# Kernel tuning notes

Measured on AMD Instinct MI355X. Metric: run time of the kernel, lower is better.

Reference implementation:

```python
import jax, jax.numpy as jnp
import numpy as np

HIDDEN = 2048
HEADS = 16
HEAD_DIM = HIDDEN // HEADS
ROPE_BASE = 10000.0


def rope_cos_sin(seq_len, dim, dtype=jnp.float32):
    inv_freq = 1.0 / (ROPE_BASE ** (jnp.arange(0, dim, 2, dtype=jnp.float32) / dim))
    t = jnp.arange(seq_len, dtype=jnp.float32)
    freqs = jnp.einsum('i,j->ij', t, inv_freq)            # [S, dim/2]
    emb = jnp.concatenate([freqs, freqs], axis=-1)        # [S, dim]
    return jnp.cos(emb).astype(dtype), jnp.sin(emb).astype(dtype)


def rotate_half(x):
    x1, x2 = jnp.split(x, 2, axis=-1)
    return jnp.concatenate([-x2, x1], axis=-1)


def setup_inputs() -> dict:
    key = jax.random.key(0)
    ks = jax.random.split(key, 6)
    B, S, D = 2, 2048, HIDDEN
    scale = 1.0 / np.sqrt(D)
    x = jax.random.normal(ks[0], (B, S, D), dtype=jnp.float32)
    Wq = jax.random.normal(ks[1], (D, D), dtype=jnp.float32) * scale
    Wk = jax.random.normal(ks[2], (D, D), dtype=jnp.float32) * scale
    Wv = jax.random.normal(ks[3], (D, D), dtype=jnp.float32) * scale
    Wo = jax.random.normal(ks[4], (D, D), dtype=jnp.float32) * scale
    bo = jnp.zeros((D,), dtype=jnp.float32)
    return {"x": x, "Wq": Wq, "Wk": Wk, "Wv": Wv, "Wo": Wo, "bo": bo}


def reference(x, Wq, Wk, Wv, Wo, bo):
    B, S, D = x.shape
    H, Dh = HEADS, HEAD_DIM
    # torch Linear: x @ W.T
    q = (x @ Wq.T).reshape(B, S, H, Dh).transpose(0, 2, 1, 3)  # [B,H,S,Dh]
    k = (x @ Wk.T).reshape(B, S, H, Dh).transpose(0, 2, 1, 3)
    v = (x @ Wv.T).reshape(B, S, H, Dh).transpose(0, 2, 1, 3)
    cos, sin = rope_cos_sin(S, Dh, x.dtype)                    # [S, Dh]
    q = q * cos + rotate_half(q) * sin
    k = k * cos + rotate_half(k) * sin
    scale = Dh ** -0.5
    attn = jnp.einsum('bhqd,bhkd->bhqk', q, k) * scale
    attn = jax.nn.softmax(attn, axis=-1)
    out = jnp.einsum('bhqk,bhkd->bhqd', attn, v)               # [B,H,S,Dh]
    out = out.transpose(0, 2, 1, 3).reshape(B, S, D)
    return out @ Wo.T + bo
```

## Files before the change

kernel.cpp:

```cpp
#include <hip/hip_runtime.h>
#include <stdint.h>


#define SEQ 2048
#define HD 128
#define DMODEL 2048

typedef __bf16 bf16x8 __attribute__((ext_vector_type(8)));
typedef float f32x4 __attribute__((ext_vector_type(4)));
typedef unsigned short u16;
typedef unsigned int u32;

typedef bf16x8 __attribute__((may_alias)) bf16x8_a;
typedef uint2 __attribute__((may_alias)) uint2_a;
typedef uint4 __attribute__((may_alias)) uint4_a;

__device__ __forceinline__ u16 f2bf(float f) {
  unsigned int u = __float_as_uint(f);
  u += 0x7fff + ((u >> 16) & 1);
  return (u16)(u >> 16);
}

typedef __attribute__((address_space(1))) void* gas_t;
typedef __attribute__((address_space(3))) void* las_t;
__device__ __forceinline__ void load_lds16(const void* g, void* l) {
  __builtin_amdgcn_global_load_lds((gas_t)(uintptr_t)g,
                                   (las_t)(uint32_t)(uintptr_t)l, 16, 0, 0);
}

__global__ void conv_all(const float* __restrict__ x,
                         const float* __restrict__ wq,
                         const float* __restrict__ wk,
                         const float* __restrict__ wv,
                         const float* __restrict__ wo,
                         u16* __restrict__ xb, u16* __restrict__ wqkv,
                         u16* __restrict__ wob) {
  int i = blockIdx.x * 256 + threadIdx.x;
  const float* src;
  u16* dst;
  int off;
  if (i < 2097152) { src = x; dst = xb; off = i; }
  else if (i < 3145728) { src = wq; dst = wqkv; off = i - 2097152; }
  else if (i < 4194304) { src = wk; dst = wqkv + 4194304; off = i - 3145728; }
  else if (i < 5242880) { src = wv; dst = wqkv + 8388608; off = i - 4194304; }
  else { src = wo; dst = wob; off = i - 5242880; }
  float4 v = ((const float4*)src)[off];
  ushort4 o;
  o.x = f2bf(v.x); o.y = f2bf(v.y); o.z = f2bf(v.z); o.w = f2bf(v.w);
  ((ushort4*)dst)[off] = o;
}


#define BARR asm volatile("s_barrier" ::: "memory")
#define LGKM0 asm volatile("s_waitcnt lgkmcnt(0)" ::: "memory")
#define VMW2 asm volatile("s_waitcnt vmcnt(2)" ::: "memory")
#define VMW8 asm volatile("s_waitcnt vmcnt(8)" ::: "memory")
#define VMW0 asm volatile("s_waitcnt vmcnt(0)" ::: "memory")

#define STGA(D, KOFF) do {                                                  \
    const u16* ga_ = Ag + (KOFF);                                           \
    u16* la_ = S + (D) * 16384;                                             \
    load_lds16(ga_ + off[0], la_ + tid * 8);                                \
    load_lds16(ga_ + off[1], la_ + (tid + 512) * 8);                        \
    load_lds16(ga_ + off[2], la_ + (tid + 1024) * 8);                       \
    load_lds16(ga_ + off[3], la_ + (tid + 1536) * 8);                       \
  } while (0)

#define STGB(D, KOFF) do {                                                  \
    const u16* gb_ = Bg + (KOFF);                                           \
    u16* lb_ = S + 32768 + (D) * 8192;                                      \
    load_lds16(gb_ + off[0], lb_ + tid * 8);                                \
    load_lds16(gb_ + off[1], lb_ + (tid + 512) * 8);                        \
  } while (0)

#define LDA2(D, MH) do {                                                    \
    const u16* ab_ = S + (D) * 16384;                                       \
    _Pragma("unroll") for (int mt_ = 0; mt_ < 2; ++mt_) {                   \
      int rA_ = wm * 64 + ((MH) * 2 + mt_) * 16 + l15;                      \
      int sw_ = rA_ & 7;                                                    \
      af[mt_][0] = *(const bf16x8_a*)(ab_ + (rA_ * 8 + (quad ^ sw_)) * 8);  \
      af[mt_][1] = *(const bf16x8_a*)(ab_ + (rA_ * 8 + ((4 + quad) ^ sw_)) * 8); \
    } } while (0)

#define LDB2(D) do {                                                        \
    const u16* bb_ = S + 32768 + (D) * 8192;                                \
    _Pragma("unroll") for (int nt_ = 0; nt_ < 4; ++nt_) {                   \
      int rB_ = wn * 64 + nt_ * 16 + l15;                                   \
      int sw_ = rB_ & 7;                                                    \
      bfr[nt_][0] = *(const bf16x8_a*)(bb_ + (rB_ * 8 + (quad ^ sw_)) * 8); \
      bfr[nt_][1] = *(const bf16x8_a*)(bb_ + (rB_ * 8 + ((4 + quad) ^ sw_)) * 8); \
    } } while (0)

#define MM2(MH) do {                                                        \
    __builtin_amdgcn_s_setprio(1);                                          \
    _Pragma("unroll") for (int c_ = 0; c_ < 2; ++c_)                        \
      _Pragma("unroll") for (int mt_ = 0; mt_ < 2; ++mt_)                   \
        _Pragma("unroll") for (int nt_ = 0; nt_ < 4; ++nt_) {               \
          if (VM)                                                           \
            acc[(MH) * 2 + mt_][nt_] =                                      \
                __builtin_amdgcn_mfma_f32_16x16x32_bf16(                    \
                    bfr[nt_][c_], af[mt_][c_],                              \
                    acc[(MH) * 2 + mt_][nt_], 0, 0, 0);                     \
          else                                                              \
            acc[(MH) * 2 + mt_][nt_] =                                      \
                __builtin_amdgcn_mfma_f32_16x16x32_bf16(                    \
                    af[mt_][c_], bfr[nt_][c_],                              \
                    acc[(MH) * 2 + mt_][nt_], 0, 0, 0);                     \
        }                                                                   \
    __builtin_amdgcn_s_setprio(0);                                          \
  } while (0)

template <bool VM>
__device__ __forceinline__ void mm_core(const u16* __restrict__ Ag,
                                        const u16* __restrict__ Bg,
                                        u16* __restrict__ S, int tid,
                                        f32x4 acc[4][4]) {
  const int lane = tid & 63;
  const int wave = tid >> 6;
  const int quad = lane >> 4;
  const int l15 = lane & 15;
  const int wm = wave >> 1;
  const int wn = wave & 1;

  u32 off[4];
#pragma unroll
  for (int j = 0; j < 4; ++j) {
    int idx = tid + j * 512;
    int r = idx >> 3;
    off[j] = (u32)r * 2048u + (u32)(((idx & 7) ^ (r & 7)) * 8);
  }

  bf16x8 af[2][2], bfr[4][2];

  STGA(0, 0);
  STGB(0, 0);
  STGB(1, 64);
  VMW2;
  BARR;

#pragma unroll 2
  for (int t = 0; t < 32; ++t) {
    const int d = t & 1;
    LDA2(d, 0); LDB2(d);
    if (t < 31) STGA(1 - d, (t + 1) * 64);
    BARR; LGKM0; MM2(0); BARR;
    LDA2(d, 1);
    if (t < 30) STGB(d, (t + 2) * 64);
    BARR; LGKM0; MM2(1);
    if (t < 30) { VMW2; } else if (t == 30) { VMW0; }
    BARR;
  }
}

__global__ __launch_bounds__(512, 2)
void gemm_qkv(const u16* __restrict__ A, const u16* __restrict__ Bm,
              u16* __restrict__ qkv, u16* __restrict__ vt) {
  __shared__ __align__(16) u16 S[49152];

  const int tid = threadIdx.x;
  int hwid = blockIdx.y * 48 + blockIdx.x;
  int logical = (hwid & 7) * 96 + (hwid >> 3);
  const int bx = logical >> 4;
  const int by = logical & 15;
  const int row0 = by * 256;
  const int col0 = bx * 128;
  const bool vmode = bx >= 32;

  const u16* Ag = A + (size_t)row0 * 2048;
  const u16* Bg = Bm + (size_t)col0 * 2048;

  f32x4 acc[4][4] = {};
  if (vmode) mm_core<true>(Ag, Bg, S, tid, acc);
  else       mm_core<false>(Ag, Bg, S, tid, acc);

  const int lane = tid & 63;
  const int wave = tid >> 6;
  const int quad = lane >> 4;
  const int l15 = lane & 15;
  const int wm = wave >> 1;
  const int wn = wave & 1;

  const int which = bx >> 4;
  const int h = bx & 15;
  const int brow = row0 >> 11;
  const int sbase = row0 & 2047;
  const float qs = (which == 0) ? 0.12751744f : 1.0f;

#pragma unroll
  for (int mt = 0; mt < 4; ++mt)
#pragma unroll
    for (int nt = 0; nt < 4; ++nt)
#pragma unroll
      for (int r = 0; r < 4; ++r) {
        int el;
        if (vmode) {
          int dd = wn * 64 + nt * 16 + quad * 4 + r;
          int ss = wm * 64 + mt * 16 + l15;
          el = dd * 256 + (((ss >> 3) ^ (dd & 31)) * 8) + (ss & 7);
        } else {
          int ss = wm * 64 + mt * 16 + quad * 4 + r;
          int dd = wn * 64 + nt * 16 + l15;
          el = ss * 128 + (((dd >> 3) ^ (ss & 15)) * 8) + (dd & 7);
        }
        S[el] = f2bf(acc[mt][nt][r] * qs);
      }
  __syncthreads();

  if (!vmode) {
    const int a = lane & 7;
    const int sg = lane >> 3;
    const float c1 = 0.2076205059304601f;
    const float c2 = 2.6514961294723187f;
#pragma unroll
    for (int pass = 0; pass < 4; ++pass) {
      int s_l = pass * 64 + wave * 8 + sg;
      int s2048 = sbase + s_l;
      int sw = s_l & 15;
      bf16x8 x1 = *(const bf16x8_a*)&S[s_l * 128 + ((a ^ sw) * 8)];
      bf16x8 x2 = *(const bf16x8_a*)&S[s_l * 128 + (((a + 8) ^ sw) * 8)];
      u16 o1[8], o2[8];
#pragma unroll
      for (int e = 0; e < 8; ++e) {
        float j = (float)(a * 8 + e);
        float rev = (float)s2048 * __builtin_amdgcn_exp2f(-c1 * j - c2);
        rev = __builtin_amdgcn_fractf(rev);
        float sn = __builtin_amdgcn_sinf(rev);
        float cs = __builtin_amdgcn_cosf(rev);
        float v1 = (float)x1[e], v2 = (float)x2[e];
        o1[e] = f2bf(v1 * cs - v2 * sn);
        o2[e] = f2bf(v2 * cs + v1 * sn);
      }
      size_t base =
          ((((size_t)which * 2 + brow) * 16 + h) * SEQ + s2048) * HD + a * 8;
      *(uint4_a*)&qkv[base] = *(uint4*)o1;
      *(uint4_a*)&qkv[base + 64] = *(uint4*)o2;
    }
  } else {
    const int d_part = tid >> 4;
    const int a0 = tid & 15;
#pragma unroll
    for (int pass = 0; pass < 4; ++pass) {
      int d_l = pass * 32 + d_part;
      int dw = d_l & 31;
      size_t rb = (((size_t)brow * 16 + h) * HD + d_l) * SEQ + sbase;
#pragma unroll
      for (int g = 0; g < 2; ++g) {
        int a2 = a0 + g * 16;
        bf16x8 y = *(const bf16x8_a*)&S[d_l * 256 + ((a2 ^ dw) * 8)];
        *(uint4_a*)&vt[rb + a2 * 8] = *(uint4_a*)&y;
      }
    }
  }
}

__global__ __launch_bounds__(512, 2)
void gemm_out(const u16* __restrict__ A, const u16* __restrict__ Bm,
              float* __restrict__ C, const float* __restrict__ bias) {
  __shared__ __align__(16) u16 S[49152];

  const int tid = threadIdx.x;
  int hwid = blockIdx.y * 16 + blockIdx.x;
  int logical = (hwid & 7) * 32 + (hwid >> 3);
  const int bx = logical >> 4;
  const int by = logical & 15;
  const int row0 = by * 256;
  const int col0 = bx * 128;

  const u16* Ag = A + (size_t)row0 * 2048;
  const u16* Bg = Bm + (size_t)col0 * 2048;

  f32x4 acc[4][4] = {};
  mm_core<false>(Ag, Bg, S, tid, acc);

  const int lane = tid & 63;
  const int wave = tid >> 6;
  const int quad = lane >> 4;
  const int l15 = lane & 15;
  const int wm = wave >> 1;
  const int wn = wave & 1;

#pragma unroll
  for (int nt = 0; nt < 4; ++nt) {
    int d = col0 + wn * 64 + nt * 16 + l15;
    float bv = bias[d];
#pragma unroll
    for (int mt = 0; mt < 4; ++mt) {
#pragma unroll
      for (int r = 0; r < 4; ++r) {
        int row = row0 + wm * 64 + mt * 16 + quad * 4 + r;
        C[(size_t)row * DMODEL + d] = acc[mt][nt][r] + bv;
      }
    }
  }
}

__global__ __launch_bounds__(256, 2)
void attn_kernel(const u16* __restrict__ qkv, const u16* __restrict__ vt,
                 u16* __restrict__ attn_out) {
  __shared__ __align__(16) u16 Kl[2][64 * 128];
  __shared__ __align__(16) u16 Vl[2][128 * 64];
  __shared__ __align__(16) u16 Pl[4][32 * 64];

  const int tid = threadIdx.x;
  const int lane = tid & 63;
  const int wave = tid >> 6;
  const int quad = lane >> 4;
  const int l15 = lane & 15;
  const int q0 = blockIdx.x * 128;
  const int bh = blockIdx.y;
  const size_t SD = (size_t)SEQ * HD;

  const u16* Q = qkv + (size_t)bh * SD;
  const u16* Kg = qkv + (size_t)(32 + bh) * SD;
  const u16* Vg = vt + (size_t)bh * SD;

  bf16x8 onesf;
#pragma unroll
  for (int e = 0; e < 8; ++e)
    onesf[e] = (l15 == 0) ? (__bf16)1.0f : (__bf16)0.0f;

  bf16x8 qf[2][4];
#pragma unroll
  for (int mt = 0; mt < 2; ++mt) {
    int qrow = q0 + wave * 32 + mt * 16 + l15;
#pragma unroll
    for (int c = 0; c < 4; ++c)
      qf[mt][c] = *(const bf16x8*)(Q + (size_t)qrow * HD + c * 32 + quad * 8);
  }

  f32x4 of[9][2] = {};
  u16* pw = &Pl[wave][0];

  auto stage = [&](int tile, int buf) {
    int kv0 = tile * 64;
#pragma unroll
    for (int j = 0; j < 4; ++j) {
      int idx = (wave * 4 + j) * 64 + lane;
      {
        int r = idx >> 4, cs = idx & 15;
        int cc = cs ^ (r & 15);
        load_lds16(Kg + (size_t)(kv0 + r) * HD + cc * 8, &Kl[buf][idx * 8]);
      }
      {
        int r = idx >> 3, cs = idx & 7;
        int cc = cs ^ (r & 7);
        load_lds16(Vg + (size_t)r * SEQ + kv0 + cc * 8, &Vl[buf][idx * 8]);
      }
    }
  };

  stage(0, 0);
  stage(1, 1);
  VMW8;
  BARR;

#pragma unroll 2
  for (int t = 0; t < 32; ++t) {
    const u16* Kb = Kl[t & 1];
    const u16* Vb = Vl[t & 1];

    f32x4 sc[4][2] = {};
    __builtin_amdgcn_s_setprio(1);
#pragma unroll
    for (int c = 0; c < 4; ++c) {
      bf16x8 kf[4];
#pragma unroll
      for (int nt = 0; nt < 4; ++nt)
        kf[nt] = *(const bf16x8*)&Kb[((nt * 16 + l15) * 16 +
                                      ((c * 4 + quad) ^ l15)) * 8];
#pragma unroll
      for (int nt = 0; nt < 4; ++nt)
#pragma unroll
        for (int mt = 0; mt < 2; ++mt)
          sc[nt][mt] = __builtin_amdgcn_mfma_f32_16x16x32_bf16(
              kf[nt], qf[mt][c], sc[nt][mt], 0, 0, 0);
    }
    __builtin_amdgcn_s_setprio(0);

#pragma unroll
    for (int nt = 0; nt < 4; ++nt) {
#pragma unroll
      for (int mt = 0; mt < 2; ++mt) {
        float p0 = __builtin_amdgcn_exp2f(sc[nt][mt][0]);
        float p1 = __builtin_amdgcn_exp2f(sc[nt][mt][1]);
        float p2 = __builtin_amdgcn_exp2f(sc[nt][mt][2]);
        float p3 = __builtin_amdgcn_exp2f(sc[nt][mt][3]);
        u32 lo = __builtin_amdgcn_perm(__float_as_uint(p1),
                                       __float_as_uint(p0), 0x07060302u);
        u32 hi = __builtin_amdgcn_perm(__float_as_uint(p3),
                                       __float_as_uint(p2), 0x07060302u);
        int row = mt * 16 + l15;
        int a = nt * 2 + (quad >> 1);
        int idx16 = (row * 8 + (a ^ (l15 & 7))) * 8 + (quad & 1) * 4;
        uint2 pk; pk.x = lo; pk.y = hi;
        *(uint2_a*)&pw[idx16] = pk;
      }
    }

    __builtin_amdgcn_s_setprio(1);
#pragma unroll
    for (int c = 0; c < 2; ++c) {
      bf16x8 pf[2];
#pragma unroll
      for (int mt = 0; mt < 2; ++mt)
        pf[mt] = *(const bf16x8_a*)&pw[((mt * 16 + l15) * 8 +
                                        ((c * 4 + quad) ^ (l15 & 7))) * 8];
#pragma unroll
      for (int dt = 0; dt < 9; ++dt) {
        bf16x8 vf = (dt < 8)
                        ? *(const bf16x8*)&Vb[((dt * 16 + l15) * 8 +
                                               ((c * 4 + quad) ^ (l15 & 7))) * 8]
                        : onesf;
#pragma unroll
        for (int mt = 0; mt < 2; ++mt)
          of[dt][mt] = __builtin_amdgcn_mfma_f32_16x16x32_bf16(
              vf, pf[mt], of[dt][mt], 0, 0, 0);
      }
    }
    __builtin_amdgcn_s_setprio(0);

    BARR;
    if (t < 30) {
      stage(t + 2, t & 1);
      VMW8;
    } else {
      VMW0;
    }
    BARR;
  }

  const int b = bh >> 4, h = bh & 15;
#pragma unroll
  for (int mt = 0; mt < 2; ++mt) {
    float lsum = __shfl(of[8][mt][0], l15, 64);
    float inv = 1.f / lsum;
    int s = q0 + wave * 32 + mt * 16 + l15;
    size_t rowb = ((size_t)b * SEQ + s) * DMODEL + h * HD;
#pragma unroll
    for (int dt = 0; dt < 8; ++dt) {
      ushort4 ov;
      ov.x = f2bf(of[dt][mt][0] * inv);
      ov.y = f2bf(of[dt][mt][1] * inv);
      ov.z = f2bf(of[dt][mt][2] * inv);
      ov.w = f2bf(of[dt][mt][3] * inv);
      *(ushort4*)&attn_out[rowb + dt * 16 + quad * 4] = ov;
    }
  }
}

extern "C" void kernel_launch(void* const* d_in, const int* in_sizes, int n_in,
                              void* d_out, int out_size, void* d_ws,
                              size_t ws_size, hipStream_t stream) {
  const float* x = (const float*)d_in[0];
  const float* Wq = (const float*)d_in[1];
  const float* Wk = (const float*)d_in[2];
  const float* Wv = (const float*)d_in[3];
  const float* Wo = (const float*)d_in[4];
  const float* bo = (const float*)d_in[5];
  float* out = (float*)d_out;

  char* ws = (char*)d_ws;
  u16* xb = (u16*)(ws);
  u16* wqkv = (u16*)(ws + (size_t)(16 << 20));
  u16* wob = (u16*)(ws + (size_t)(40 << 20));
  u16* qkv = (u16*)(ws + (size_t)(48 << 20));
  u16* vt = qkv + (size_t)2 * 8388608;
  u16* attn = xb;

  conv_all<<<24576, 256, 0, stream>>>(x, Wq, Wk, Wv, Wo, xb, wqkv, wob);

  gemm_qkv<<<dim3(48, 16), 512, 0, stream>>>(xb, wqkv, qkv, vt);
  attn_kernel<<<dim3(16, 32), 256, 0, stream>>>(qkv, vt, attn);
  gemm_out<<<dim3(16, 16), 512, 0, stream>>>(attn, wob, out, bo);
}
```

Before: 358.9 us.

## Triple-buffer LDS stages in GEMM mainloop with deeper prefetch

Converts the shared GEMM core from a two-stage to a three-stage LDS pipeline, prefetching A and B tiles two k-steps ahead. The loop is unrolled by three with an explicit tail, and the wait count is relaxed to keep more global loads in flight. This enlarges the shared memory per block to 144KB, which may reduce the number of resident blocks per CU below the requested two.

```diff
diff --git a/kernel.cpp b/kernel.cpp
--- a/kernel.cpp
+++ b/kernel.cpp
@@ -53,7 +53,7 @@
 
 #define BARR asm volatile("s_barrier" ::: "memory")
 #define LGKM0 asm volatile("s_waitcnt lgkmcnt(0)" ::: "memory")
-#define VMW2 asm volatile("s_waitcnt vmcnt(2)" ::: "memory")
+#define VMW6 asm volatile("s_waitcnt vmcnt(6)" ::: "memory")
 #define VMW8 asm volatile("s_waitcnt vmcnt(8)" ::: "memory")
 #define VMW0 asm volatile("s_waitcnt vmcnt(0)" ::: "memory")
 
@@ -68,7 +68,7 @@
 
 #define STGB(D, KOFF) do {                                                  \
     const u16* gb_ = Bg + (KOFF);                                           \
-    u16* lb_ = S + 32768 + (D) * 8192;                                      \
+    u16* lb_ = S + 49152 + (D) * 8192;                                      \
     load_lds16(gb_ + off[0], lb_ + tid * 8);                                \
     load_lds16(gb_ + off[1], lb_ + (tid + 512) * 8);                        \
   } while (0)
@@ -83,7 +83,7 @@
     } } while (0)
 
 #define LDB2(D) do {                                                        \
-    const u16* bb_ = S + 32768 + (D) * 8192;                                \
+    const u16* bb_ = S + 49152 + (D) * 8192;                                \
     _Pragma("unroll") for (int nt_ = 0; nt_ < 4; ++nt_) {                   \
       int rB_ = wn * 64 + nt_ * 16 + l15;                                   \
       int sw_ = rB_ & 7;                                                    \
@@ -110,6 +110,15 @@
     __builtin_amdgcn_s_setprio(0);                                          \
   } while (0)
 
+#define STEP3(T, CUR, NX2) do {                                             \
+    LDA2(CUR, 0); LDB2(CUR);                                                \
+    STGA(NX2, ((T) + 2) * 64);                                              \
+    BARR; LGKM0; MM2(0); BARR;                                              \
+    LDA2(CUR, 1);                                                           \
+    STGB(NX2, ((T) + 2) * 64);                                              \
+    BARR; LGKM0; MM2(1); VMW6; BARR;                                        \
+  } while (0)
+
 template <bool VM>
 __device__ __forceinline__ void mm_core(const u16* __restrict__ Ag,
                                         const u16* __restrict__ Bg,
@@ -134,28 +143,32 @@
 
   STGA(0, 0);
   STGB(0, 0);
+  STGA(1, 64);
   STGB(1, 64);
-  VMW2;
+  VMW6;
   BARR;
 
-#pragma unroll 2
-  for (int t = 0; t < 32; ++t) {
-    const int d = t & 1;
-    LDA2(d, 0); LDB2(d);
-    if (t < 31) STGA(1 - d, (t + 1) * 64);
-    BARR; LGKM0; MM2(0); BARR;
-    LDA2(d, 1);
-    if (t < 30) STGB(d, (t + 2) * 64);
-    BARR; LGKM0; MM2(1);
-    if (t < 30) { VMW2; } else if (t == 30) { VMW0; }
-    BARR;
-  }
+#pragma unroll 1
+  for (int tt = 0; tt < 30; tt += 3) {
+    STEP3(tt,     0, 2);
+    STEP3(tt + 1, 1, 0);
+    STEP3(tt + 2, 2, 1);
+  }
+
+  LDA2(0, 0); LDB2(0);
+  BARR; LGKM0; MM2(0); BARR;
+  LDA2(0, 1);
+  BARR; LGKM0; MM2(1); VMW0; BARR;
+  LDA2(1, 0); LDB2(1);
+  BARR; LGKM0; MM2(0); BARR;
+  LDA2(1, 1);
+  BARR; LGKM0; MM2(1); BARR;
 }
 
 __global__ __launch_bounds__(512, 2)
 void gemm_qkv(const u16* __restrict__ A, const u16* __restrict__ Bm,
               u16* __restrict__ qkv, u16* __restrict__ vt) {
-  __shared__ __align__(16) u16 S[49152];
+  __shared__ __align__(16) u16 S[73728];
 
   const int tid = threadIdx.x;
   int hwid = blockIdx.y * 48 + blockIdx.x;
@@ -256,7 +269,7 @@
 __global__ __launch_bounds__(512, 2)
 void gemm_out(const u16* __restrict__ A, const u16* __restrict__ Bm,
               float* __restrict__ C, const float* __restrict__ bias) {
-  __shared__ __align__(16) u16 S[49152];
+  __shared__ __align__(16) u16 S[73728];
 
   const int tid = threadIdx.x;
   int hwid = blockIdx.y * 16 + blockIdx.x;
```

Measured after the change: 356.5 us. About the same (-0.7%).

## Triple-buffer GEMM mainloop with K=32 tiles and raise occupancy bound

Applied to the files above, without the earlier changes.

The shared GEMM core drops from a double-buffered K=64 tile with several barriers and lgkm waits per iteration to a triple-buffered K=32 pipeline. Each step loads fragments, issues the global-to-LDS copies two tiles ahead, runs 16 MFMAs, then waits once and hits one barrier. The LDS swizzle is redone for 32-wide rows and LDS per block shrinks. Launch bounds rise to 4 blocks per CU, which may cap registers and force spills of the 64-float accumulator. The smaller K tile also means more barriers overall.

```diff
diff --git a/kernel.cpp b/kernel.cpp
--- a/kernel.cpp
+++ b/kernel.cpp
@@ -52,62 +52,57 @@
 
 
 #define BARR asm volatile("s_barrier" ::: "memory")
-#define LGKM0 asm volatile("s_waitcnt lgkmcnt(0)" ::: "memory")
-#define VMW2 asm volatile("s_waitcnt vmcnt(2)" ::: "memory")
+#define VMW3 asm volatile("s_waitcnt vmcnt(3)" ::: "memory")
 #define VMW8 asm volatile("s_waitcnt vmcnt(8)" ::: "memory")
 #define VMW0 asm volatile("s_waitcnt vmcnt(0)" ::: "memory")
 
-#define STGA(D, KOFF) do {                                                  \
+#define STGA32(D, KOFF) do {                                                \
     const u16* ga_ = Ag + (KOFF);                                           \
-    u16* la_ = S + (D) * 16384;                                             \
-    load_lds16(ga_ + off[0], la_ + tid * 8);                                \
-    load_lds16(ga_ + off[1], la_ + (tid + 512) * 8);                        \
-    load_lds16(ga_ + off[2], la_ + (tid + 1024) * 8);                       \
-    load_lds16(ga_ + off[3], la_ + (tid + 1536) * 8);                       \
+    u16* la_ = S + (D) * 8192;                                              \
+    load_lds16(ga_ + offA0, la_ + tid * 8);                                 \
+    load_lds16(ga_ + offA1, la_ + (tid + 512) * 8);                         \
   } while (0)
 
-#define STGB(D, KOFF) do {                                                  \
+#define STGB32(D, KOFF) do {                                                \
     const u16* gb_ = Bg + (KOFF);                                           \
-    u16* lb_ = S + 32768 + (D) * 8192;                                      \
-    load_lds16(gb_ + off[0], lb_ + tid * 8);                                \
-    load_lds16(gb_ + off[1], lb_ + (tid + 512) * 8);                        \
+    u16* lb_ = S + 24576 + (D) * 4096;                                      \
+    load_lds16(gb_ + offA0, lb_ + tid * 8);                                 \
   } while (0)
 
-#define LDA2(D, MH) do {                                                    \
-    const u16* ab_ = S + (D) * 16384;                                       \
-    _Pragma("unroll") for (int mt_ = 0; mt_ < 2; ++mt_) {                   \
-      int rA_ = wm * 64 + ((MH) * 2 + mt_) * 16 + l15;                      \
-      int sw_ = rA_ & 7;                                                    \
-      af[mt_][0] = *(const bf16x8_a*)(ab_ + (rA_ * 8 + (quad ^ sw_)) * 8);  \
-      af[mt_][1] = *(const bf16x8_a*)(ab_ + (rA_ * 8 + ((4 + quad) ^ sw_)) * 8); \
-    } } while (0)
-
-#define LDB2(D) do {                                                        \
-    const u16* bb_ = S + 32768 + (D) * 8192;                                \
+#define LDAB32(D) do {                                                      \
+    const u16* ab_ = S + (D) * 8192;                                        \
+    const u16* bb_ = S + 24576 + (D) * 4096;                                \
+    _Pragma("unroll") for (int mt_ = 0; mt_ < 4; ++mt_) {                   \
+      int rA_ = wm * 64 + mt_ * 16 + l15;                                   \
+      af[mt_] = *(const bf16x8_a*)(ab_ + rA_ * 32 +                         \
+                                   ((quad ^ ((rA_ >> 1) & 3)) * 8));        \
+    }                                                                       \
     _Pragma("unroll") for (int nt_ = 0; nt_ < 4; ++nt_) {                   \
       int rB_ = wn * 64 + nt_ * 16 + l15;                                   \
-      int sw_ = rB_ & 7;                                                    \
-      bfr[nt_][0] = *(const bf16x8_a*)(bb_ + (rB_ * 8 + (quad ^ sw_)) * 8); \
-      bfr[nt_][1] = *(const bf16x8_a*)(bb_ + (rB_ * 8 + ((4 + quad) ^ sw_)) * 8); \
+      bfr[nt_] = *(const bf16x8_a*)(bb_ + rB_ * 32 +                        \
+                                    ((quad ^ ((rB_ >> 1) & 3)) * 8));       \
     } } while (0)
 
-#define MM2(MH) do {                                                        \
+#define MM32() do {                                                         \
     __builtin_amdgcn_s_setprio(1);                                          \
-    _Pragma("unroll") for (int c_ = 0; c_ < 2; ++c_)                        \
-      _Pragma("unroll") for (int mt_ = 0; mt_ < 2; ++mt_)                   \
-        _Pragma("unroll") for (int nt_ = 0; nt_ < 4; ++nt_) {               \
-          if (VM)                                                           \
-            acc[(MH) * 2 + mt_][nt_] =                                      \
-                __builtin_amdgcn_mfma_f32_16x16x32_bf16(                    \
-                    bfr[nt_][c_], af[mt_][c_],                              \
-                    acc[(MH) * 2 + mt_][nt_], 0, 0, 0);                     \
-          else                                                              \
-            acc[(MH) * 2 + mt_][nt_] =                                      \
-                __builtin_amdgcn_mfma_f32_16x16x32_bf16(                    \
-                    af[mt_][c_], bfr[nt_][c_],                              \
-                    acc[(MH) * 2 + mt_][nt_], 0, 0, 0);                     \
-        }                                                                   \
+    _Pragma("unroll") for (int mt_ = 0; mt_ < 4; ++mt_)                     \
+      _Pragma("unroll") for (int nt_ = 0; nt_ < 4; ++nt_) {                 \
+        if (VM)                                                             \
+          acc[mt_][nt_] = __builtin_amdgcn_mfma_f32_16x16x32_bf16(          \
+              bfr[nt_], af[mt_], acc[mt_][nt_], 0, 0, 0);                   \
+        else                                                                \
+          acc[mt_][nt_] = __builtin_amdgcn_mfma_f32_16x16x32_bf16(          \
+              af[mt_], bfr[nt_], acc[mt_][nt_], 0, 0, 0);                   \
+      }                                                                     \
     __builtin_amdgcn_s_setprio(0);                                          \
+  } while (0)
+
+#define STEP32(T, CUR, NX2) do {                                            \
+    LDAB32(CUR);                                                            \
+    STGA32(NX2, ((T) + 2) * 32);                                            \
+    STGB32(NX2, ((T) + 2) * 32);                                            \
+    MM32();                                                                 \
+    VMW3; BARR;                                                             \
   } while (0)
 
 template <bool VM>
@@ -122,40 +117,55 @@
   const int wm = wave >> 1;
   const int wn = wave & 1;
 
-  u32 off[4];
-#pragma unroll
-  for (int j = 0; j < 4; ++j) {
-    int idx = tid + j * 512;
-    int r = idx >> 3;
-    off[j] = (u32)r * 2048u + (u32)(((idx & 7) ^ (r & 7)) * 8);
-  }
-
-  bf16x8 af[2][2], bfr[4][2];
-
-  STGA(0, 0);
-  STGB(0, 0);
-  STGB(1, 64);
-  VMW2;
+  u32 offA0, offA1;
+  {
+    int r = tid >> 2;
+    offA0 = (u32)r * 2048u + (u32)((((tid & 3) ^ ((r >> 1) & 3)) * 8));
+  }
+  {
+    int i1 = tid + 512;
+    int r = i1 >> 2;
+    offA1 = (u32)r * 2048u + (u32)((((i1 & 3) ^ ((r >> 1) & 3)) * 8));
+  }
+
+  bf16x8 af[4], bfr[4];
+
+  STGA32(0, 0);
+  STGB32(0, 0);
+  STGA32(1, 32);
+  STGB32(1, 32);
+  VMW3;
   BARR;
 
-#pragma unroll 2
-  for (int t = 0; t < 32; ++t) {
-    const int d = t & 1;
-    LDA2(d, 0); LDB2(d);
-    if (t < 31) STGA(1 - d, (t + 1) * 64);
-    BARR; LGKM0; MM2(0); BARR;
-    LDA2(d, 1);
-    if (t < 30) STGB(d, (t + 2) * 64);
-    BARR; LGKM0; MM2(1);
-    if (t < 30) { VMW2; } else if (t == 30) { VMW0; }
-    BARR;
-  }
-}
-
-__global__ __launch_bounds__(512, 2)
+#pragma unroll 1
+  for (int tt = 0; tt < 60; tt += 3) {
+    STEP32(tt,     0, 2);
+    STEP32(tt + 1, 1, 0);
+    STEP32(tt + 2, 2, 1);
+  }
+
+  LDAB32(0);
+  STGA32(2, 62 * 32);
+  STGB32(2, 62 * 32);
+  MM32();
+  VMW3; BARR;
+  LDAB32(1);
+  STGA32(0, 63 * 32);
+  STGB32(0, 63 * 32);
+  MM32();
+  VMW3; BARR;
+  LDAB32(2);
+  MM32();
+  VMW0; BARR;
+  LDAB32(0);
+  MM32();
+  BARR;
+}
+
+__global__ __launch_bounds__(512, 4)
 void gemm_qkv(const u16* __restrict__ A, const u16* __restrict__ Bm,
               u16* __restrict__ qkv, u16* __restrict__ vt) {
-  __shared__ __align__(16) u16 S[49152];
+  __shared__ __align__(16) u16 S[36864];
 
   const int tid = threadIdx.x;
   int hwid = blockIdx.y * 48 + blockIdx.x;
@@ -253,10 +263,10 @@
   }
 }
 
-__global__ __launch_bounds__(512, 2)
+__global__ __launch_bounds__(512, 4)
 void gemm_out(const u16* __restrict__ A, const u16* __restrict__ Bm,
               float* __restrict__ C, const float* __restrict__ bias) {
-  __shared__ __align__(16) u16 S[49152];
+  __shared__ __align__(16) u16 S[36864];
 
   const int tid = threadIdx.x;
   int hwid = blockIdx.y * 16 + blockIdx.x;
```

Measured after the change: 365.0 us. No clear change (+1.7%).
